# Performance work log

Measured on AMD Instinct MI355X. Metric: run time of the kernel, lower is better.

## Reference

```python
import jax, jax.numpy as jnp
import numpy as np
from jax import lax

B, F, I, S = 4, 1024, 2048, 2048
K, G = 7, 4
INIT_SCALE = 1.0
LEAK = 0.02


def _norm(x):
    # normalize over channel dim (axis 1): subtract mean, divide by RMS-style L2 norm
    x = x - jnp.mean(x, axis=1, keepdims=True)
    n = jnp.sqrt(jnp.sum(x * x, axis=1, keepdims=True)) * (x.shape[1] ** -0.5)
    return x / (n + 1e-5)


def _conv1x1(x, w):
    # x: [B, Cin, S], w: [Cout, Cin, 1]
    return jnp.einsum('bcs,oc->bos', x, w[:, :, 0])


def setup_inputs() -> dict:
    key = jax.random.key(0)
    k1, k2, k3, k4 = jax.random.split(key, 4)
    inp = jax.random.normal(k1, (B, F, S), dtype=jnp.float32)
    divisor = (jnp.arange(S, dtype=jnp.float32) + 1.0).reshape(1, 1, S)
    w0_gate = jax.random.normal(k2, (3 * I, F, 1), dtype=jnp.float32) * (F ** -0.5)
    w1 = jax.random.normal(k3, (3 * I, I // G, K), dtype=jnp.float32) * ((I // G * K) ** -0.5)
    w2_gate = jax.random.normal(k4, (F, I, 1), dtype=jnp.float32) * (I ** -0.5)
    return {"inp": inp, "divisor": divisor, "w0_gate": w0_gate, "w1": w1, "w2_gate": w2_gate}


def reference(inp, divisor, w0_gate, w1, w2_gate):
    # 1x1 conv features -> 3*intermediate
    x = _conv1x1(inp, w0_gate)                       # [B, 3I, S]
    depth, scale, shift = jnp.split(x, 3, axis=1)    # each [B, I, S]
    cum = jnp.cumsum(depth, axis=-1)
    x = jax.nn.leaky_relu(_norm(cum / divisor * scale + shift), LEAK)
    # causal pad + grouped conv1d intermediate -> 3*intermediate
    x = jnp.pad(x, ((0, 0), (0, 0), (K - 1, 0)))
    x = lax.conv_general_dilated(x, w1, window_strides=(1,), padding='VALID',
                                 dimension_numbers=('NCH', 'OIH', 'NCH'),
                                 feature_group_count=G)  # [B, 3I, S]
    s0, s1, sh = jnp.split(x, 3, axis=1)
    x = jax.nn.leaky_relu(_norm(s0 * s1 + sh), LEAK)     # [B, I, S]
    # 1x1 conv intermediate -> features
    out = _conv1x1(x, w2_gate)                           # [B, F, S]
    return out * INIT_SCALE
```

## Files before the change

### kernel.cpp

```cpp
#include <hip/hip_runtime.h>

#define BATCH 4
#define FDIM  1024
#define IDIM  2048
#define SDIM  2048
#define I3    6144
#define KW    7
#define IG    512
#define OG    1536
#define KD2   3584
#define SP    2056

using short8 = __attribute__((ext_vector_type(8))) short;
using f32x4  = __attribute__((ext_vector_type(4))) float;

__device__ __forceinline__ unsigned short f2bf(float f) {
  unsigned int u = __float_as_uint(f);
  u += 0x7fffu + ((u >> 16) & 1u);
  return (unsigned short)(u >> 16);
}
__device__ __forceinline__ float bf2f(unsigned short u) {
  return __uint_as_float((unsigned int)u << 16);
}

__device__ __forceinline__ void gload16(const void* g, void* l) {
  __builtin_amdgcn_global_load_lds((const __attribute__((address_space(1))) void*)g,
                                   (__attribute__((address_space(3))) void*)l,
                                   16, 0, 0);
}

template<int MODE, int OBF16>
__global__ __launch_bounds__(512, 1)
void gemm256(const unsigned short* __restrict__ A,
             const unsigned short* __restrict__ Bt,
             void* __restrict__ C,
             int mtiles, int ktiles,
             int lda, int ldb, int ldc,
             long aZ, long bZ, long cZ)
{
  __shared__ unsigned short lds[2][2][16384];

  const int tid  = threadIdx.x;
  const int wv   = tid >> 6;
  const int lane = tid & 63;
  const int lr = lane & 15, lq = lane >> 4;
  const int wr = wv >> 2, wc = wv & 3;
  const int xm = (lr & 7) << 4;
  const int c8 = ((tid & 7) ^ ((tid >> 3) & 7)) << 3;

  const int nwg = gridDim.x;
  const int cpx = nwg >> 3;
  const int bid = blockIdx.x;
  const int w   = (bid & 7) * cpx + (bid >> 3);
  const int T   = mtiles << 3;
  const int z   = w / T;
  const int rr  = w - z * T;
  const int mt  = rr % mtiles;
  const int nt  = rr / mtiles;

  const unsigned short* Ab;
  const unsigned short* Bb;
  size_t coff;
  int gbase = 0;
  if (MODE == 2) {
    int b = z >> 2, g = z & 3;
    Ab = A + (size_t)g * OG * KD2;
    Bb = Bt + (size_t)b * SP * IDIM;
    coff = ((size_t)b * I3 + (size_t)g * OG) * (size_t)ldc;
    gbase = g * IG;
  } else {
    Ab = A + (size_t)z * aZ;
    Bb = Bt + (size_t)z * bZ;
    coff = (size_t)z * cZ;
  }

  const int m0 = mt * 256, n0 = nt * 256;

  f32x4 acc[8][4];
  const f32x4 vzero = {0.f, 0.f, 0.f, 0.f};
#pragma unroll
  for (int i = 0; i < 8; ++i)
#pragma unroll
    for (int j = 0; j < 4; ++j) acc[i][j] = vzero;

  auto STAGE = [&](int buf, int kt1) {
    const int k0 = kt1 << 6;
#pragma unroll
    for (int t = 0; t < 4; ++t) {
      int row = (t << 6) + (tid >> 3);
      gload16(Ab + (size_t)(m0 + row) * lda + (k0 + c8),
              &lds[buf][0][t * 4096 + wv * 512]);
    }
#pragma unroll
    for (int t = 0; t < 4; ++t) {
      int row = (t << 6) + (tid >> 3);
      const unsigned short* g;
      if (MODE == 2) {
        int kk = k0 + c8;
        g = Bb + (size_t)(n0 + row + (kk >> 9) + 2) * IDIM + (gbase + (kk & 511));
      } else {
        g = Bb + (size_t)(n0 + row) * ldb + (k0 + c8);
      }
      gload16(g, &lds[buf][1][t * 4096 + wv * 512]);
    }
  };

  auto RDA = [&](int buf, int i, int kk) -> short8 {
    int row = wr * 128 + i * 16 + lr;
    int off = ((row << 7) + (kk << 1) + (lq << 4)) ^ xm;
    return *(const short8*)((const char*)&lds[buf][0][0] + off);
  };
  auto RDB = [&](int buf, int j, int kk) -> short8 {
    int row = wc * 64 + j * 16 + lr;
    int off = ((row << 7) + (kk << 1) + (lq << 4)) ^ xm;
    return *(const short8*)((const char*)&lds[buf][1][0] + off);
  };

  STAGE(0, 0);
  asm volatile("s_waitcnt vmcnt(0)" ::: "memory");
  __builtin_amdgcn_s_barrier();
  __builtin_amdgcn_sched_barrier(0);

  for (int kt = 0; kt < ktiles; ++kt) {
    const int cur = kt & 1;
    if (kt + 1 < ktiles) STAGE(cur ^ 1, kt + 1);
    __builtin_amdgcn_sched_barrier(0);

    __builtin_amdgcn_s_setprio(1);
#pragma unroll
    for (int kh = 0; kh < 2; ++kh) {
      const int kk = kh * 32;
      short8 bfv[4], af[8];
#pragma unroll
      for (int j = 0; j < 4; ++j) bfv[j] = RDB(cur, j, kk);
#pragma unroll
      for (int i = 0; i < 8; ++i) af[i] = RDA(cur, i, kk);
#pragma unroll
      for (int i = 0; i < 8; ++i)
#pragma unroll
        for (int j = 0; j < 4; ++j)
          acc[i][j] = __builtin_amdgcn_mfma_f32_16x16x32_bf16(af[i], bfv[j], acc[i][j], 0, 0, 0);
    }
    __builtin_amdgcn_s_setprio(0);

    asm volatile("s_waitcnt vmcnt(0)" ::: "memory");
    __builtin_amdgcn_s_barrier();
    __builtin_amdgcn_sched_barrier(0);
  }

#pragma unroll
  for (int i = 0; i < 8; ++i) {
#pragma unroll
    for (int j = 0; j < 4; ++j) {
      int ccol  = n0 + wc * 64 + j * 16 + lr;
      int rbase = m0 + wr * 128 + i * 16 + lq * 4;
      if (OBF16) {
        unsigned short* Cs = (unsigned short*)C + coff;
#pragma unroll
        for (int e = 0; e < 4; ++e)
          Cs[(size_t)(rbase + e) * ldc + ccol] = f2bf(acc[i][j][e]);
      } else {
        float* Cf = (float*)C + coff;
#pragma unroll
        for (int e = 0; e < 4; ++e)
          Cf[(size_t)(rbase + e) * ldc + ccol] = acc[i][j][e];
      }
    }
  }
}

__global__ void cvt_f2b(const float* __restrict__ in, unsigned short* __restrict__ out, long n) {
  long stride = (long)gridDim.x * blockDim.x;
  for (long i = (long)blockIdx.x * blockDim.x + threadIdx.x; i < n; i += stride)
    out[i] = f2bf(in[i]);
}

__global__ void perm_w1(const float* __restrict__ in, unsigned short* __restrict__ out) {
  const long n = (long)I3 * KD2;
  long stride = (long)gridDim.x * blockDim.x;
  for (long idx = (long)blockIdx.x * blockDim.x + threadIdx.x; idx < n; idx += stride) {
    long o  = idx / KD2;
    int rem = (int)(idx - o * KD2);
    int k   = rem >> 9;
    int c   = rem & 511;
    out[idx] = f2bf(in[o * KD2 + (long)c * KW + k]);
  }
}

__global__ void transpose_in(const float* __restrict__ in, unsigned short* __restrict__ out) {
  __shared__ float tile[64][65];
  int bid = blockIdx.x;
  int b   = bid >> 9;
  int rem = bid & 511;
  int ft  = rem >> 5;
  int st  = rem & 31;
  int tc  = threadIdx.x & 63, tr = threadIdx.x >> 6;
  const float* ip = in + ((size_t)b * FDIM + ft * 64) * SDIM + st * 64;
#pragma unroll
  for (int r = tr; r < 64; r += 4)
    tile[r][tc] = ip[(size_t)r * SDIM + tc];
  __syncthreads();
  unsigned short* op = out + ((size_t)b * SDIM + st * 64) * FDIM + ft * 64;
#pragma unroll
  for (int r = tr; r < 64; r += 4)
    op[(size_t)r * FDIM + tc] = f2bf(tile[tc][r]);
}

__global__ void scan_rows(const unsigned short* __restrict__ C1, unsigned short* __restrict__ V) {
  int rid = blockIdx.x;
  int b = rid >> 11;
  int i = rid & 2047;
  const unsigned short* dp = C1 + ((size_t)b * I3 + i) * SDIM;
  const unsigned short* sp = dp + (size_t)IDIM * SDIM;
  const unsigned short* hp = dp + (size_t)2 * IDIM * SDIM;
  unsigned short* vp = V + ((size_t)b * IDIM + i) * SDIM;
  int t = threadIdx.x;

  short8 dv = *(const short8*)(dp + t * 8);
  float c[8];
  float run = 0.f;
#pragma unroll
  for (int e = 0; e < 8; ++e) { run += bf2f((unsigned short)dv[e]); c[e] = run; }

  __shared__ float ps[256];
  ps[t] = run;
  __syncthreads();
  for (int off = 1; off < 256; off <<= 1) {
    float vv = (t >= off) ? ps[t - off] : 0.f;
    __syncthreads();
    ps[t] += vv;
    __syncthreads();
  }
  float excl = ps[t] - run;

  short8 sv = *(const short8*)(sp + t * 8);
  short8 hv = *(const short8*)(hp + t * 8);
  short8 ov;
#pragma unroll
  for (int e = 0; e < 8; ++e) {
    int s = t * 8 + e;
    float val = (excl + c[e]) / (float)(s + 1) * bf2f((unsigned short)sv[e]) + bf2f((unsigned short)hv[e]);
    ov[e] = (short)f2bf(val);
  }
  *(short8*)(vp + t * 8) = ov;
}

template<int MODE>
__global__ void stats_part(const unsigned short* __restrict__ X, float* __restrict__ psum,
                           float* __restrict__ psq) {
  int bid = blockIdx.x;
  int b   = bid >> 5;
  int s0  = (bid & 31) * 64;
  int iz  = blockIdx.y;
  int ts  = threadIdx.x & 63, tg = threadIdx.x >> 6;
  float sum = 0.f, sq = 0.f;
  for (int i = iz * 512 + tg; i < iz * 512 + 512; i += 4) {
    float g;
    if (MODE == 1) {
      g = bf2f(X[((size_t)b * IDIM + i) * SDIM + s0 + ts]);
    } else {
      float a  = bf2f(X[((size_t)b * I3 + i) * SDIM + s0 + ts]);
      float bb = bf2f(X[((size_t)b * I3 + IDIM + i) * SDIM + s0 + ts]);
      float cc = bf2f(X[((size_t)b * I3 + 2 * IDIM + i) * SDIM + s0 + ts]);
      g = a * bb + cc;
    }
    sum += g; sq += g * g;
  }
  __shared__ float sS[4][64], sQ[4][64];
  sS[tg][ts] = sum; sQ[tg][ts] = sq;
  __syncthreads();
  if (threadIdx.x < 64) {
    float s = sS[0][ts] + sS[1][ts] + sS[2][ts] + sS[3][ts];
    float q = sQ[0][ts] + sQ[1][ts] + sQ[2][ts] + sQ[3][ts];
    psum[((size_t)b * SDIM + s0 + ts) * 4 + iz] = s;
    psq [((size_t)b * SDIM + s0 + ts) * 4 + iz] = q;
  }
}

__global__ void stats_final(const float* __restrict__ psum, const float* __restrict__ psq,
                            float* __restrict__ mean, float* __restrict__ inv) {
  int idx = blockIdx.x * 256 + threadIdx.x;
  if (idx >= BATCH * SDIM) return;
  float s = psum[idx * 4] + psum[idx * 4 + 1] + psum[idx * 4 + 2] + psum[idx * 4 + 3];
  float q = psq [idx * 4] + psq [idx * 4 + 1] + psq [idx * 4 + 2] + psq [idx * 4 + 3];
  float m   = s * (1.f / 2048.f);
  float var = q * (1.f / 2048.f) - m * m;
  float n   = sqrtf(fmaxf(var, 0.f));
  mean[idx] = m;
  inv[idx]  = 1.f / (n + 1e-5f);
}

template<int MODE>
__global__ void norm_apply(const unsigned short* __restrict__ X, const float* __restrict__ mean,
                           const float* __restrict__ inv, unsigned short* __restrict__ out) {
  __shared__ float tile[64][65];
  int bid = blockIdx.x;
  int b   = bid >> 5;
  int s0  = (bid & 31) * 64;
  int i0  = blockIdx.y * 512;
  int tc  = threadIdx.x & 63, tr = threadIdx.x >> 6;
  float mn = mean[(size_t)b * SDIM + s0 + tc];
  float iv = inv [(size_t)b * SDIM + s0 + tc];
  size_t orow = (MODE == 1) ? ((size_t)b * SP + 8 + s0) : ((size_t)b * SDIM + s0);
  for (int ic = i0; ic < i0 + 512; ic += 64) {
#pragma unroll
    for (int r = tr; r < 64; r += 4) {
      int i = ic + r;
      float g;
      if (MODE == 1) {
        g = bf2f(X[((size_t)b * IDIM + i) * SDIM + s0 + tc]);
      } else {
        float a  = bf2f(X[((size_t)b * I3 + i) * SDIM + s0 + tc]);
        float bb = bf2f(X[((size_t)b * I3 + IDIM + i) * SDIM + s0 + tc]);
        float cc = bf2f(X[((size_t)b * I3 + 2 * IDIM + i) * SDIM + s0 + tc]);
        g = a * bb + cc;
      }
      float y = (g - mn) * iv;
      y = (y >= 0.f) ? y : 0.02f * y;
      tile[r][tc] = y;
    }
    __syncthreads();
#pragma unroll
    for (int r = tr; r < 64; r += 4)
      out[(orow + r) * IDIM + ic + tc] = f2bf(tile[tc][r]);
    __syncthreads();
  }
}

__global__ void zero_x1t_pad(unsigned short* __restrict__ x1t) {
  int idx = blockIdx.x * 256 + threadIdx.x;
  if (idx < BATCH * 8 * IDIM) {
    int b   = idx / (8 * IDIM);
    int rem = idx - b * (8 * IDIM);
    x1t[(size_t)b * SP * IDIM + rem] = 0;
  }
}

__global__ void report_ws(float* __restrict__ out, float mb) {
  if (threadIdx.x == 0 && blockIdx.x == 0) out[0] = mb;
}

extern "C" void kernel_launch(void* const* d_in, const int* in_sizes, int n_in,
                              void* d_out, int out_size, void* d_ws, size_t ws_size,
                              hipStream_t stream) {
  const float* inp = (const float*)d_in[0];
  const float* w0  = (const float*)d_in[2];
  const float* w1  = (const float*)d_in[3];
  const float* w2  = (const float*)d_in[4];
  float* out = (float*)d_out;
  char* ws = (char*)d_ws;

  const size_t REQ = 216465408ULL;
  if (ws_size < REQ) {
    report_ws<<<1, 1, 0, stream>>>(out, (float)(ws_size >> 20));
    return;
  }

  unsigned short* A2   = (unsigned short*)(ws + 0);
  unsigned short* A3   = (unsigned short*)(ws + 44040192);
  unsigned short* C1   = (unsigned short*)(ws + 48234496);
  unsigned short* X1T  = (unsigned short*)(ws + 148897792);
  char*           VXr  = ws + 182583296;
  unsigned short* A1   = (unsigned short*)(VXr + 0);
  unsigned short* BINT = (unsigned short*)(VXr + 12582912);
  unsigned short* V    = (unsigned short*)(VXr + 0);
  unsigned short* X2T  = (unsigned short*)(VXr + 0);
  float* PSUM = (float*)(ws + 216137728);
  float* PSQ  = (float*)(ws + 216268800);
  float* MEAN = (float*)(ws + 216399872);
  float* INV  = (float*)(ws + 216432640);

  cvt_f2b<<<2048, 256, 0, stream>>>(w0, A1, (long)I3 * FDIM);
  cvt_f2b<<<2048, 256, 0, stream>>>(w2, A3, (long)FDIM * IDIM);
  perm_w1<<<4096, 256, 0, stream>>>(w1, A2);
  transpose_in<<<2048, 256, 0, stream>>>(inp, BINT);
  zero_x1t_pad<<<256, 256, 0, stream>>>(X1T);

  gemm256<0, 1><<<24 * 8 * BATCH, 512, 0, stream>>>(
      A1, BINT, C1, 24, 16, FDIM, FDIM, SDIM,
      0L, (long)SDIM * FDIM, (long)I3 * SDIM);

  scan_rows<<<BATCH * IDIM, 256, 0, stream>>>(C1, V);

  stats_part<1><<<dim3(128, 4), 256, 0, stream>>>(V, PSUM, PSQ);
  stats_final<<<32, 256, 0, stream>>>(PSUM, PSQ, MEAN, INV);
  norm_apply<1><<<dim3(128, 4), 256, 0, stream>>>(V, MEAN, INV, X1T);

  gemm256<2, 1><<<6 * 8 * 16, 512, 0, stream>>>(
      A2, X1T, C1, 6, 56, KD2, 0, SDIM, 0L, 0L, 0L);

  stats_part<2><<<dim3(128, 4), 256, 0, stream>>>(C1, PSUM, PSQ);
  stats_final<<<32, 256, 0, stream>>>(PSUM, PSQ, MEAN, INV);
  norm_apply<2><<<dim3(128, 4), 256, 0, stream>>>(C1, MEAN, INV, X2T);

  gemm256<0, 0><<<4 * 8 * BATCH, 512, 0, stream>>>(
      A3, X2T, out, 4, 32, IDIM, IDIM, SDIM,
      0L, (long)SDIM * IDIM, (long)FDIM * SDIM);
}
```

Measured before the change: 697.0 us.

## Interleave global prefetch chunks and LDS reads with MFMA groups in GEMM main loop

Splits the next-tile global-to-LDS staging into four chunks and interleaves them with four MFMA groups and double-buffered register fragments, so loads, LDS reads and matrix ops overlap within each k-tile. The last iteration is peeled so the loop runs without a prefetch branch. This targets stalls where MFMAs waited on LDS reads and global issue sat in one burst. It raises register pressure and depends on how the compiler schedules the interleaving, which could hurt occupancy.

```diff
diff --git a/kernel.cpp b/kernel.cpp
--- a/kernel.cpp
+++ b/kernel.cpp
@@ -83,26 +83,19 @@
 #pragma unroll
     for (int j = 0; j < 4; ++j) acc[i][j] = vzero;
 
-  auto STAGE = [&](int buf, int kt1) {
+  auto STAGEC = [&](int buf, int kt1, int c) {
     const int k0 = kt1 << 6;
-#pragma unroll
-    for (int t = 0; t < 4; ++t) {
-      int row = (t << 6) + (tid >> 3);
-      gload16(Ab + (size_t)(m0 + row) * lda + (k0 + c8),
-              &lds[buf][0][t * 4096 + wv * 512]);
+    int row = (c << 6) + (tid >> 3);
+    gload16(Ab + (size_t)(m0 + row) * lda + (k0 + c8),
+            &lds[buf][0][c * 4096 + wv * 512]);
+    const unsigned short* g;
+    if (MODE == 2) {
+      int kk = k0 + c8;
+      g = Bb + (size_t)(n0 + row + (kk >> 9) + 2) * IDIM + (gbase + (kk & 511));
+    } else {
+      g = Bb + (size_t)(n0 + row) * ldb + (k0 + c8);
     }
-#pragma unroll
-    for (int t = 0; t < 4; ++t) {
-      int row = (t << 6) + (tid >> 3);
-      const unsigned short* g;
-      if (MODE == 2) {
-        int kk = k0 + c8;
-        g = Bb + (size_t)(n0 + row + (kk >> 9) + 2) * IDIM + (gbase + (kk & 511));
-      } else {
-        g = Bb + (size_t)(n0 + row) * ldb + (k0 + c8);
-      }
-      gload16(g, &lds[buf][1][t * 4096 + wv * 512]);
-    }
+    gload16(g, &lds[buf][1][c * 4096 + wv * 512]);
   };
 
   auto RDA = [&](int buf, int i, int kk) -> short8 {
@@ -116,37 +109,72 @@
     return *(const short8*)((const char*)&lds[buf][1][0] + off);
   };
 
-  STAGE(0, 0);
+#define MFMA16(AF, BV, IOFF)                                                     \
+  __builtin_amdgcn_s_setprio(1);                                                 \
+  _Pragma("unroll")                                                              \
+  for (int i = 0; i < 4; ++i)                                                    \
+    _Pragma("unroll")                                                            \
+    for (int j = 0; j < 4; ++j)                                                  \
+      acc[i + IOFF][j] =                                                         \
+          __builtin_amdgcn_mfma_f32_16x16x32_bf16(AF[i], BV[j], acc[i + IOFF][j],\
+                                                  0, 0, 0);                      \
+  __builtin_amdgcn_s_setprio(0);
+
+  STAGEC(0, 0, 0); STAGEC(0, 0, 1); STAGEC(0, 0, 2); STAGEC(0, 0, 3);
   asm volatile("s_waitcnt vmcnt(0)" ::: "memory");
   __builtin_amdgcn_s_barrier();
   __builtin_amdgcn_sched_barrier(0);
 
-  for (int kt = 0; kt < ktiles; ++kt) {
+  for (int kt = 0; kt < ktiles - 1; ++kt) {
     const int cur = kt & 1;
-    if (kt + 1 < ktiles) STAGE(cur ^ 1, kt + 1);
-    __builtin_amdgcn_sched_barrier(0);
-
-    __builtin_amdgcn_s_setprio(1);
-#pragma unroll
-    for (int kh = 0; kh < 2; ++kh) {
-      const int kk = kh * 32;
-      short8 bfv[4], af[8];
-#pragma unroll
-      for (int j = 0; j < 4; ++j) bfv[j] = RDB(cur, j, kk);
-#pragma unroll
-      for (int i = 0; i < 8; ++i) af[i] = RDA(cur, i, kk);
-#pragma unroll
-      for (int i = 0; i < 8; ++i)
-#pragma unroll
-        for (int j = 0; j < 4; ++j)
-          acc[i][j] = __builtin_amdgcn_mfma_f32_16x16x32_bf16(af[i], bfv[j], acc[i][j], 0, 0, 0);
-    }
-    __builtin_amdgcn_s_setprio(0);
+    short8 af0[4], af1[4], bv0[4], bv1[4];
+#pragma unroll
+    for (int j = 0; j < 4; ++j) bv0[j] = RDB(cur, j, 0);
+#pragma unroll
+    for (int i = 0; i < 4; ++i) af0[i] = RDA(cur, i, 0);
+    STAGEC(cur ^ 1, kt + 1, 0);
+#pragma unroll
+    for (int i = 0; i < 4; ++i) af1[i] = RDA(cur, i + 4, 0);
+    MFMA16(af0, bv0, 0)
+    STAGEC(cur ^ 1, kt + 1, 1);
+#pragma unroll
+    for (int j = 0; j < 4; ++j) bv1[j] = RDB(cur, j, 32);
+#pragma unroll
+    for (int i = 0; i < 4; ++i) af0[i] = RDA(cur, i, 32);
+    MFMA16(af1, bv0, 4)
+    STAGEC(cur ^ 1, kt + 1, 2);
+#pragma unroll
+    for (int i = 0; i < 4; ++i) af1[i] = RDA(cur, i + 4, 32);
+    MFMA16(af0, bv1, 0)
+    STAGEC(cur ^ 1, kt + 1, 3);
+    MFMA16(af1, bv1, 4)
 
     asm volatile("s_waitcnt vmcnt(0)" ::: "memory");
     __builtin_amdgcn_s_barrier();
     __builtin_amdgcn_sched_barrier(0);
   }
+
+  {
+    const int cur = (ktiles - 1) & 1;
+    short8 af0[4], af1[4], bv0[4], bv1[4];
+#pragma unroll
+    for (int j = 0; j < 4; ++j) bv0[j] = RDB(cur, j, 0);
+#pragma unroll
+    for (int i = 0; i < 4; ++i) af0[i] = RDA(cur, i, 0);
+#pragma unroll
+    for (int i = 0; i < 4; ++i) af1[i] = RDA(cur, i + 4, 0);
+    MFMA16(af0, bv0, 0)
+#pragma unroll
+    for (int j = 0; j < 4; ++j) bv1[j] = RDB(cur, j, 32);
+#pragma unroll
+    for (int i = 0; i < 4; ++i) af0[i] = RDA(cur, i, 32);
+    MFMA16(af1, bv0, 4)
+#pragma unroll
+    for (int i = 0; i < 4; ++i) af1[i] = RDA(cur, i + 4, 32);
+    MFMA16(af0, bv1, 0)
+    MFMA16(af1, bv1, 4)
+  }
+#undef MFMA16
 
 #pragma unroll
   for (int i = 0; i < 8; ++i) {
```

New measurement: 690.4 us. About the same (-1.0%).
